# Performance work log

Measured on AMD Instinct MI355X. Metric: run time of the kernel, lower is better.

The kernel has to match this reference:

```python
import jax, jax.numpy as jnp
import numpy as np
from jax import lax

EPS = 1e-5
NUM_GROUPS = 32
OFFSET_SCALE = 1.0
K = 3            # deformable conv kernel size
KK = K * K
DWK = 7          # depthwise kernel size for offset predictor


def group_norm(x, gamma, beta, num_groups=NUM_GROUPS):
    B, C, H, W = x.shape
    xg = x.reshape(B, num_groups, C // num_groups, H, W)
    m = xg.mean(axis=(2, 3, 4), keepdims=True)
    v = xg.var(axis=(2, 3, 4), keepdims=True)
    xn = ((xg - m) * lax.rsqrt(v + EPS)).reshape(B, C, H, W)
    return xn * gamma[None, :, None, None] + beta[None, :, None, None]


def bilinear_gather(x, py, px):
    # x: [B,C,H,W]; py, px: [B,KK,H,W] absolute sample coords -> [B,C,KK,H,W]
    B, C, H, W = x.shape
    y0 = jnp.floor(py)
    x0 = jnp.floor(px)
    wy1 = py - y0
    wx1 = px - x0
    wy0 = 1.0 - wy1
    wx0 = 1.0 - wx1
    xf = x.reshape(B, C, H * W)

    def gather(yi, xi):
        valid = (yi >= 0) & (yi <= H - 1) & (xi >= 0) & (xi <= W - 1)
        yc = jnp.clip(yi, 0, H - 1).astype(jnp.int32)
        xc = jnp.clip(xi, 0, W - 1).astype(jnp.int32)
        idx = (yc * W + xc).reshape(B, -1)                      # [B, KK*H*W]
        g = jax.vmap(lambda a, i: a[:, i])(xf, idx)             # [B, C, KK*H*W]
        g = g.reshape(B, C, KK, H, W)
        return g * valid.astype(x.dtype)[:, None]

    out = (gather(y0, x0) * (wy0 * wx0)[:, None]
           + gather(y0, x0 + 1.0) * (wy0 * wx1)[:, None]
           + gather(y0 + 1.0, x0) * (wy1 * wx0)[:, None]
           + gather(y0 + 1.0, x0 + 1.0) * (wy1 * wx1)[:, None])
    return out


def deform_conv(x, dw, pw, pwb, w, b):
    # x: [B,C,H,W]; dw: [C,1,DWK,DWK] depthwise; pw: [2*KK,C,1,1]; w: [O,C,K,K]
    B, C, H, W = x.shape
    dn = ('NCHW', 'OIHW', 'NCHW')
    f = lax.conv_general_dilated(x, dw, (1, 1), 'SAME',
                                 feature_group_count=C, dimension_numbers=dn)
    off = lax.conv_general_dilated(f, pw, (1, 1), 'SAME', dimension_numbers=dn)
    off = (off + pwb[None, :, None, None]) * OFFSET_SCALE       # [B,2*KK,H,W]
    off = off.reshape(B, KK, 2, H, W)
    ks = jnp.arange(K, dtype=x.dtype) - (K - 1) / 2             # [-1,0,1]
    ky = jnp.repeat(ks, K)                                      # [KK]
    kx = jnp.tile(ks, K)
    yy, xx = jnp.meshgrid(jnp.arange(H, dtype=x.dtype),
                          jnp.arange(W, dtype=x.dtype), indexing='ij')
    py = yy[None, None] + ky[None, :, None, None] + off[:, :, 0]  # [B,KK,H,W]
    px = xx[None, None] + kx[None, :, None, None] + off[:, :, 1]
    sampled = bilinear_gather(x, py, px)                        # [B,C,KK,H,W]
    O = w.shape[0]
    out = jnp.einsum('bckhw,ock->bohw', sampled, w.reshape(O, C, KK))
    return out + b[None, :, None, None]


def setup_inputs() -> dict:
    key = jax.random.key(0)
    ks = jax.random.split(key, 10)
    B, C, H, W = 4, 256, 64, 64
    O = C
    x = jax.random.normal(ks[0], (B, C, H, W), dtype=jnp.float32)

    def conv_w(k, shape, fan_in):
        return jax.random.normal(k, shape, dtype=jnp.float32) / np.sqrt(fan_in)

    inp = {
        'x': x,
        'gn1_g': jnp.ones((C,), jnp.float32), 'gn1_b': jnp.zeros((C,), jnp.float32),
        'dw1': conv_w(ks[1], (C, 1, DWK, DWK), DWK * DWK),
        'pw1': jax.random.normal(ks[2], (2 * KK, C, 1, 1), jnp.float32) * 0.01,
        'pwb1': jnp.zeros((2 * KK,), jnp.float32),
        'w1': conv_w(ks[3], (O, C, K, K), C * KK),
        'b1': jnp.zeros((O,), jnp.float32),
        'gn2_g': jnp.ones((O,), jnp.float32), 'gn2_b': jnp.zeros((O,), jnp.float32),
        'dw2': conv_w(ks[4], (O, 1, DWK, DWK), DWK * DWK),
        'pw2': jax.random.normal(ks[5], (2 * KK, O, 1, 1), jnp.float32) * 0.01,
        'pwb2': jnp.zeros((2 * KK,), jnp.float32),
        'w2': conv_w(ks[6], (O, O, K, K), O * KK),
        'b2': jnp.zeros((O,), jnp.float32),
    }
    return inp


def reference(x, gn1_g, gn1_b, dw1, pw1, pwb1, w1, b1,
              gn2_g, gn2_b, dw2, pw2, pwb2, w2, b2):
    h = jax.nn.relu(group_norm(x, gn1_g, gn1_b))
    h = deform_conv(h, dw1, pw1, pwb1, w1, b1)
    h = jax.nn.relu(group_norm(h, gn2_g, gn2_b))
    # Dropout / DropPath are identity in eval mode
    h = deform_conv(h, dw2, pw2, pwb2, w2, b2)
    return h + x  # shortcut is Identity (in_channels == out_channels)
```

## Files before the change

kernel.cpp:

```cpp
#include <hip/hip_runtime.h>

#define B_    4
#define C_    256
#define H_    64
#define W_    64
#define HW_   4096
#define NG_   32
#define CPG_  8
#define KK_   9
#define NOFF_ 18

typedef __attribute__((ext_vector_type(8))) short short8;
typedef __attribute__((ext_vector_type(4))) short short4v;
typedef __attribute__((ext_vector_type(4))) float floatx4;
typedef __attribute__((ext_vector_type(16))) float floatx16;

static __device__ __forceinline__ short f2bf(float f) {
    union { float f; unsigned u; } v; v.f = f;
    unsigned r = v.u + 0x7fff + ((v.u >> 16) & 1);
    return (short)(r >> 16);
}
static __device__ __forceinline__ float bf2f(short s) {
    union { unsigned u; float f; } v;
    v.u = ((unsigned)(unsigned short)s) << 16;
    return v.f;
}
static __device__ __forceinline__ unsigned pkbf(float lo, float hi) {
    unsigned r;
    asm("v_cvt_pk_bf16_f32 %0, %1, %2" : "=v"(r) : "v"(lo), "v"(hi));
    return r;
}

__global__ __launch_bounds__(1024) void gn_relu_f32_kernel(
    const float* __restrict__ in, const float* __restrict__ gamma,
    const float* __restrict__ beta, short* __restrict__ outb)
{
    int b = blockIdx.x >> 5;
    int g = blockIdx.x & 31;
    const int N = CPG_ * HW_;
    size_t base = ((size_t)(b * C_ + g * CPG_)) * HW_;
    const float4* in4 = (const float4*)(in + base);
    int t = threadIdx.x;

    float s = 0.f, ss = 0.f;
    for (int i = t; i < N / 4; i += 1024) {
        float4 v = in4[i];
        s  += v.x + v.y + v.z + v.w;
        ss += v.x * v.x + v.y * v.y + v.z * v.z + v.w * v.w;
    }
    #pragma unroll
    for (int off = 32; off > 0; off >>= 1) {
        s  += __shfl_down(s, off, 64);
        ss += __shfl_down(ss, off, 64);
    }
    __shared__ float red[32];
    __shared__ float sh_rs, sh_m;
    int wid = t >> 6;
    if ((t & 63) == 0) { red[wid] = s; red[16 + wid] = ss; }
    __syncthreads();
    if (t == 0) {
        float S = 0.f, SS = 0.f;
        #pragma unroll
        for (int i = 0; i < 16; ++i) { S += red[i]; SS += red[16 + i]; }
        float m = S / (float)N;
        float var = SS / (float)N - m * m;
        sh_rs = rsqrtf(var + 1e-5f);
        sh_m = m;
    }
    __syncthreads();
    float rs = sh_rs, m = sh_m;
    short4v* out4 = (short4v*)(outb + base);
    for (int i = t; i < N / 4; i += 1024) {
        int ch = g * CPG_ + (i >> 10);
        float ga = gamma[ch] * rs;
        float be = beta[ch] - m * ga;
        float4 v = in4[i];
        short4v o;
        o.x = f2bf(fmaxf(fmaf(v.x, ga, be), 0.f));
        o.y = f2bf(fmaxf(fmaf(v.y, ga, be), 0.f));
        o.z = f2bf(fmaxf(fmaf(v.z, ga, be), 0.f));
        o.w = f2bf(fmaxf(fmaf(v.w, ga, be), 0.f));
        out4[i] = o;
    }
}

__global__ __launch_bounds__(1024) void gn_relu_bf16_kernel(
    const short* __restrict__ in, const float* __restrict__ gamma,
    const float* __restrict__ beta, short* __restrict__ outb)
{
    int b = blockIdx.x >> 5;
    int g = blockIdx.x & 31;
    const int N = CPG_ * HW_;
    size_t base = ((size_t)(b * C_ + g * CPG_)) * HW_;
    const short4v* in4 = (const short4v*)(in + base);
    int t = threadIdx.x;

    float s = 0.f, ss = 0.f;
    for (int i = t; i < N / 4; i += 1024) {
        short4v sv = in4[i];
        float vx = bf2f(sv.x), vy = bf2f(sv.y), vz = bf2f(sv.z), vw = bf2f(sv.w);
        s  += vx + vy + vz + vw;
        ss += vx * vx + vy * vy + vz * vz + vw * vw;
    }
    #pragma unroll
    for (int off = 32; off > 0; off >>= 1) {
        s  += __shfl_down(s, off, 64);
        ss += __shfl_down(ss, off, 64);
    }
    __shared__ float red[32];
    __shared__ float sh_rs, sh_m;
    int wid = t >> 6;
    if ((t & 63) == 0) { red[wid] = s; red[16 + wid] = ss; }
    __syncthreads();
    if (t == 0) {
        float S = 0.f, SS = 0.f;
        #pragma unroll
        for (int i = 0; i < 16; ++i) { S += red[i]; SS += red[16 + i]; }
        float m = S / (float)N;
        float var = SS / (float)N - m * m;
        sh_rs = rsqrtf(var + 1e-5f);
        sh_m = m;
    }
    __syncthreads();
    float rs = sh_rs, m = sh_m;
    short4v* out4 = (short4v*)(outb + base);
    for (int i = t; i < N / 4; i += 1024) {
        int ch = g * CPG_ + (i >> 10);
        float ga = gamma[ch] * rs;
        float be = beta[ch] - m * ga;
        short4v sv = in4[i];
        short4v o;
        o.x = f2bf(fmaxf(fmaf(bf2f(sv.x), ga, be), 0.f));
        o.y = f2bf(fmaxf(fmaf(bf2f(sv.y), ga, be), 0.f));
        o.z = f2bf(fmaxf(fmaf(bf2f(sv.z), ga, be), 0.f));
        o.w = f2bf(fmaxf(fmaf(bf2f(sv.w), ga, be), 0.f));
        out4[i] = o;
    }
}

__global__ __launch_bounds__(256) void dw7_kernel(
    const short* __restrict__ in, const float* __restrict__ dwk,
    short* __restrict__ out)
{
    int plane = blockIdx.x;
    int c = plane & (C_ - 1);
    const short* src = in + (size_t)plane * HW_;
    short* dst = out + (size_t)plane * HW_;
    __shared__ float tile[70 * 72];
    __shared__ float wk[49];
    int t = threadIdx.x;
    if (t < 49) wk[t] = dwk[c * 49 + t];
    for (int i = t; i < 70 * 72; i += 256) tile[i] = 0.f;
    __syncthreads();
    const short4v* src4 = (const short4v*)src;
    for (int i = t; i < HW_ / 4; i += 256) {
        short4v v = src4[i];
        int y = i >> 4, x = (i & 15) * 4;
        float* tp = &tile[(y + 3) * 72 + (x + 3)];
        tp[0] = bf2f(v.x); tp[1] = bf2f(v.y);
        tp[2] = bf2f(v.z); tp[3] = bf2f(v.w);
    }
    __syncthreads();
    #pragma unroll
    for (int it = 0; it < 4; ++it) {
        int idx = it * 256 + t;
        int y = idx >> 4;
        int x0 = (idx & 15) * 4;
        float a0 = 0.f, a1 = 0.f, a2 = 0.f, a3 = 0.f;
        #pragma unroll
        for (int dy = 0; dy < 7; ++dy) {
            const float* tr = &tile[(y + dy) * 72 + x0];
            float4 ra = *(const float4*)tr;
            float4 rb = *(const float4*)(tr + 4);
            float4 rc = *(const float4*)(tr + 8);
            float r[12] = {ra.x, ra.y, ra.z, ra.w,
                           rb.x, rb.y, rb.z, rb.w,
                           rc.x, rc.y, rc.z, rc.w};
            const float* wr = &wk[dy * 7];
            #pragma unroll
            for (int dx = 0; dx < 7; ++dx) {
                float wv = wr[dx];
                a0 = fmaf(r[dx], wv, a0);
                a1 = fmaf(r[dx + 1], wv, a1);
                a2 = fmaf(r[dx + 2], wv, a2);
                a3 = fmaf(r[dx + 3], wv, a3);
            }
        }
        short4v o;
        o.x = f2bf(a0); o.y = f2bf(a1); o.z = f2bf(a2); o.w = f2bf(a3);
        *(short4v*)&dst[y * 64 + x0] = o;
    }
}

__global__ __launch_bounds__(256) void transpose2_kernel(
    const short* __restrict__ srcA, short* __restrict__ dstA,
    const short* __restrict__ srcB, short* __restrict__ dstB)
{
    int blk = blockIdx.x;
    int h = blk >> 8;
    const short* src = h ? srcB : srcA;
    short*       dst = h ? dstB : dstA;
    int q0 = blk & 255;
    int q = ((q0 & 7) << 5) | (q0 >> 3);
    int b = q >> 6;
    int px0 = (q & 63) * 64;
    __shared__ unsigned ltile[64 * 132];
    int t = threadIdx.x;
    const short* sb = src + (size_t)b * C_ * HW_;

    int pq4 = t & 15, cphi = t >> 4;
    #pragma unroll
    for (int i = 0; i < 8; ++i) {
        int cp = i * 16 + cphi;
        const short* r0 = sb + (size_t)(2 * cp) * HW_ + px0 + pq4 * 4;
        short4v lo = *(const short4v*)r0;
        short4v hi = *(const short4v*)(r0 + HW_);
        #pragma unroll
        for (int j = 0; j < 4; ++j) {
            int pl = pq4 * 4 + j;
            unsigned wrd = (unsigned)(unsigned short)lo[j]
                         | ((unsigned)(unsigned short)hi[j] << 16);
            ltile[pl * 132 + (cp ^ ((pl & 7) << 2))] = wrd;
        }
    }
    __syncthreads();

    int co = t & 31, ph = t >> 5;
    #pragma unroll
    for (int r = 0; r < 8; ++r) {
        int pl = r * 8 + ph;
        uint4 v = *(const uint4*)&ltile[pl * 132 + ((co * 4) ^ ((pl & 7) << 2))];
        *(uint4*)(dst + ((size_t)b * HW_ + px0 + pl) * C_ + co * 8) = v;
    }
}

__global__ __launch_bounds__(256) void wpack_all_kernel(
    const float* __restrict__ w1, const float* __restrict__ w2,
    const float* __restrict__ pw1, const float* __restrict__ pw2,
    short* __restrict__ wp1, short* __restrict__ wp2,
    short* __restrict__ ppk1, short* __restrict__ ppk2)
{
    int blk = blockIdx.x;
    if (blk < 4608) {
        const float* w = (blk < 2304) ? w1 : w2;
        short* wp = (blk < 2304) ? wp1 : wp2;
        int idx = (blk % 2304) * 256 + threadIdx.x;
        int j    = idx & 7;
        int lane = (idx >> 3) & 63;
        int ot   = (idx >> 9) & 7;
        int slab = idx >> 12;
        int g = slab >> 4, cc16 = slab & 15;
        int o = ot * 32 + (lane & 31);
        int c = cc16 * 16 + (lane >> 5) * 8 + j;
        wp[idx] = f2bf(w[(size_t)(o * C_ + c) * KK_ + g]);
    } else {
        int q = blk - 4608;
        const float* pw = (q < 32) ? pw1 : pw2;
        short* ppk = (q < 32) ? ppk1 : ppk2;
        int idx = (q & 31) * 256 + threadIdx.x;
        int j = idx & 7, lane = (idx >> 3) & 63;
        int ot = (idx >> 9) & 1, sl = idx >> 10;
        int o = ot * 16 + (lane & 15);
        int k = sl * 32 + (lane >> 4) * 8 + j;
        ppk[idx] = (o < NOFF_) ? f2bf(pw[o * C_ + k]) : (short)0;
    }
}

__global__ __launch_bounds__(1024, 4) void deform_fused_kernel(
    const short* __restrict__ ht,   const short* __restrict__ fdw,
    const short* __restrict__ ppk,  const float* __restrict__ pwb,
    const short* __restrict__ wp,   const float* __restrict__ bias,
    const float* __restrict__ resid, float* __restrict__ outf,
    short* __restrict__ outb)
{
    int lb = ((blockIdx.x & 7) << 5) | (blockIdx.x >> 3);
    int b = lb >> 6;
    int row = lb & 63;
    __shared__ int   i00[576], i01[576], i10[576], i11[576];
    __shared__ float c00[576], c01[576], c10[576], c11[576];
    __shared__ __align__(16) short sbuf[2][2][8192];
    float* off_lds = (float*)&sbuf[0][0][0];
    int t = threadIdx.x;
    int wv = t >> 6, lane = t & 63;
    int pq = lane >> 4, pr = lane & 15;
    int l31 = lane & 31, hi = lane >> 5;

    if (wv < 8) {
        int ot = wv & 1, ptw = wv >> 1;
        int px = ptw * 16 + pr;
        const short8* fb8 = (const short8*)(fdw +
            ((size_t)b * HW_ + row * 64 + px) * C_);
        const short8* ap = (const short8*)ppk;
        floatx4 pacc = (floatx4){0.f, 0.f, 0.f, 0.f};
        #pragma unroll
        for (int sl = 0; sl < 8; ++sl) {
            short8 af = ap[(sl * 2 + ot) * 64 + lane];
            short8 bf = fb8[sl * 4 + pq];
            pacc = __builtin_amdgcn_mfma_f32_16x16x32_bf16(af, bf, pacc, 0, 0, 0);
        }
        #pragma unroll
        for (int r = 0; r < 4; ++r) {
            int o = ot * 16 + pq * 4 + r;
            if (o < NOFF_) off_lds[o * 64 + px] = pacc[r] + pwb[o];
        }
    }
    __syncthreads();

    if (t < 576) {
        int e = t;
        int k = e >> 6, p = e & 63;
        float offy = off_lds[(2 * k) * 64 + p];
        float offx = off_lds[(2 * k + 1) * 64 + p];
        float py = (float)row + (float)(k / 3 - 1) + offy;
        float px = (float)p   + (float)(k % 3 - 1) + offx;
        float y0f = floorf(py), x0f = floorf(px);
        float wy1 = py - y0f, wx1 = px - x0f;
        float wy0 = 1.f - wy1, wx0 = 1.f - wx1;
        float y1f = y0f + 1.f, x1f = x0f + 1.f;
        bool vy0 = (y0f >= 0.f) && (y0f <= 63.f);
        bool vy1 = (y1f >= 0.f) && (y1f <= 63.f);
        bool vx0 = (x0f >= 0.f) && (x0f <= 63.f);
        bool vx1 = (x1f >= 0.f) && (x1f <= 63.f);
        int iy0 = (int)fminf(fmaxf(y0f, 0.f), 63.f);
        int iy1 = (int)fminf(fmaxf(y1f, 0.f), 63.f);
        int ix0 = (int)fminf(fmaxf(x0f, 0.f), 63.f);
        int ix1 = (int)fminf(fmaxf(x1f, 0.f), 63.f);
        i00[e] = iy0 * 64 + ix0; i01[e] = iy0 * 64 + ix1;
        i10[e] = iy1 * 64 + ix0; i11[e] = iy1 * 64 + ix1;
        c00[e] = (vy0 && vx0) ? wy0 * wx0 : 0.f;
        c01[e] = (vy0 && vx1) ? wy0 * wx1 : 0.f;
        c10[e] = (vy1 && vx0) ? wy1 * wx0 : 0.f;
        c11[e] = (vy1 && vx1) ? wy1 * wx1 : 0.f;
    }
    __syncthreads();

    int c8a = t & 7;
    int pan = (t >> 3) & 1;
    int spx = t >> 4;
    const short* hb = ht + ((size_t)b * HW_) * C_ + pan * 128 + c8a * 8;
    const short* hb0 = hb;
    const short* hb1 = hb + 64;
    int slotA = (c8a ^ (spx & 15)) * 8;
    int slotB = ((c8a + 8) ^ (spx & 15)) * 8;
    int srow = spx * 128;

    short8 ra[4], rb[4];
    auto prefetch = [&](int g) {
        int e = g * 64 + spx;
        int a00 = i00[e], a01 = i01[e], a10 = i10[e], a11 = i11[e];
        ra[0] = *(const short8*)(hb0 + (size_t)a00 * C_);
        ra[1] = *(const short8*)(hb0 + (size_t)a01 * C_);
        ra[2] = *(const short8*)(hb0 + (size_t)a10 * C_);
        ra[3] = *(const short8*)(hb0 + (size_t)a11 * C_);
        rb[0] = *(const short8*)(hb1 + (size_t)a00 * C_);
        rb[1] = *(const short8*)(hb1 + (size_t)a01 * C_);
        rb[2] = *(const short8*)(hb1 + (size_t)a10 * C_);
        rb[3] = *(const short8*)(hb1 + (size_t)a11 * C_);
    };
    auto stage_write = [&](int g, int bi) {
        int e = g * 64 + spx;
        float w00 = c00[e], w01 = c01[e], w10 = c10[e], w11 = c11[e];
        uint4 va, vb;
        float f0, f1;
        #define BLEND(R, J) (w00 * bf2f(R[0][J]) + w01 * bf2f(R[1][J]) \
                           + w10 * bf2f(R[2][J]) + w11 * bf2f(R[3][J]))
        f0 = BLEND(ra, 0); f1 = BLEND(ra, 1); va.x = pkbf(f0, f1);
        f0 = BLEND(ra, 2); f1 = BLEND(ra, 3); va.y = pkbf(f0, f1);
        f0 = BLEND(ra, 4); f1 = BLEND(ra, 5); va.z = pkbf(f0, f1);
        f0 = BLEND(ra, 6); f1 = BLEND(ra, 7); va.w = pkbf(f0, f1);
        f0 = BLEND(rb, 0); f1 = BLEND(rb, 1); vb.x = pkbf(f0, f1);
        f0 = BLEND(rb, 2); f1 = BLEND(rb, 3); vb.y = pkbf(f0, f1);
        f0 = BLEND(rb, 4); f1 = BLEND(rb, 5); vb.z = pkbf(f0, f1);
        f0 = BLEND(rb, 6); f1 = BLEND(rb, 7); vb.w = pkbf(f0, f1);
        #undef BLEND
        short* sp = &sbuf[bi][pan][srow];
        *(uint4*)&sp[slotA] = va;
        *(uint4*)&sp[slotB] = vb;
    };

    int pairId = wv & 7;
    int half = wv >> 3;

    floatx16 acc[2];
    #pragma unroll
    for (int i = 0; i < 16; ++i) { acc[0][i] = 0.f; acc[1][i] = 0.f; }

    prefetch(0);
    stage_write(0, 0);
    prefetch(1);
    __syncthreads();

    const short8* wp8 = (const short8*)wp;
    int msk = l31 & 15;

    for (int g = 0; g < 9; ++g) {
        const short* sb = &sbuf[g & 1][half][0];
        #pragma unroll
        for (int q4 = 0; q4 < 2; ++q4) {
            short8 af[4];
            #pragma unroll
            for (int qq = 0; qq < 4; ++qq)
                af[qq] = wp8[(size_t)(((g * 16 + half * 8 + q4 * 4 + qq) * 8 + pairId) * 64 + lane)];
            #pragma unroll
            for (int qq = 0; qq < 4; ++qq) {
                int ksl = q4 * 4 + qq;
                int so = ((((ksl << 1) | hi) ^ msk) << 3);
                short8 b0 = *(const short8*)&sb[l31 * 128 + so];
                short8 b1 = *(const short8*)&sb[(32 + l31) * 128 + so];
                acc[0] = __builtin_amdgcn_mfma_f32_32x32x16_bf16(af[qq], b0, acc[0], 0, 0, 0);
                acc[1] = __builtin_amdgcn_mfma_f32_32x32x16_bf16(af[qq], b1, acc[1], 0, 0, 0);
            }
        }
        if (g + 1 < 9) {
            stage_write(g + 1, (g + 1) & 1);
            if (g + 2 < 9) prefetch(g + 2);
        }
        __syncthreads();
    }

    float* xch = (float*)&sbuf[0][0][0];
    int wreg = (pairId * 2 + half) * 1024;
    floatx16 aw = half ? acc[0] : acc[1];
    floatx4* xq = (floatx4*)xch;
    #pragma unroll
    for (int j = 0; j < 4; ++j) {
        floatx4 v = {aw[j * 4 + 0], aw[j * 4 + 1], aw[j * 4 + 2], aw[j * 4 + 3]};
        xq[(wreg >> 2) + j * 64 + lane] = v;
    }
    __syncthreads();
    int rreg = (pairId * 2 + (half ^ 1)) * 1024;
    floatx16 ac = half ? acc[1] : acc[0];
    #pragma unroll
    for (int j = 0; j < 4; ++j) {
        floatx4 v = xq[(rreg >> 2) + j * 64 + lane];
        ac[j * 4 + 0] += v.x; ac[j * 4 + 1] += v.y;
        ac[j * 4 + 2] += v.z; ac[j * 4 + 3] += v.w;
    }

    #pragma unroll
    for (int r = 0; r < 16; ++r) {
        int o = pairId * 32 + (r & 3) + 8 * (r >> 2) + 4 * hi;
        float v = ac[r] + bias[o];
        size_t ob = ((size_t)(b * C_ + o)) * HW_ + row * 64 + half * 32 + l31;
        if (outf) {
            if (resid) v += resid[ob];
            outf[ob] = v;
        } else {
            outb[ob] = f2bf(v);
        }
    }
}

extern "C" void kernel_launch(void* const* d_in, const int* in_sizes, int n_in,
                              void* d_out, int out_size, void* d_ws, size_t ws_size,
                              hipStream_t stream)
{
    const float* x     = (const float*)d_in[0];
    const float* gn1_g = (const float*)d_in[1];
    const float* gn1_b = (const float*)d_in[2];
    const float* dw1   = (const float*)d_in[3];
    const float* pw1   = (const float*)d_in[4];
    const float* pwb1  = (const float*)d_in[5];
    const float* w1    = (const float*)d_in[6];
    const float* b1    = (const float*)d_in[7];
    const float* gn2_g = (const float*)d_in[8];
    const float* gn2_b = (const float*)d_in[9];
    const float* dw2   = (const float*)d_in[10];
    const float* pw2   = (const float*)d_in[11];
    const float* pwb2  = (const float*)d_in[12];
    const float* w2    = (const float*)d_in[13];
    const float* b2    = (const float*)d_in[14];
    float* out = (float*)d_out;

    float* ws   = (float*)d_ws;
    short* y1b  = (short*)ws;
    short* hbf  = (short*)(ws + 2097152);
    short* hbt  = (short*)(ws + 4194304);
    short* fdwc = (short*)(ws + 6291456);
    short* fdwt = (short*)(ws + 8388608);
    short* wp1  = (short*)(ws + 10485760);
    short* wp2  = (short*)(ws + 10780672);
    short* ppk1 = (short*)(ws + 11075584);
    short* ppk2 = (short*)(ws + 11079680);

    wpack_all_kernel<<<4672, 256, 0, stream>>>(w1, w2, pw1, pw2,
                                               wp1, wp2, ppk1, ppk2);

    gn_relu_f32_kernel<<<B_ * NG_, 1024, 0, stream>>>(x, gn1_g, gn1_b, hbf);
    dw7_kernel<<<B_ * C_, 256, 0, stream>>>(hbf, dw1, fdwc);
    transpose2_kernel<<<512, 256, 0, stream>>>(hbf, hbt, fdwc, fdwt);
    deform_fused_kernel<<<B_ * H_, 1024, 0, stream>>>(
        hbt, fdwt, ppk1, pwb1, wp1, b1, nullptr, nullptr, y1b);

    gn_relu_bf16_kernel<<<B_ * NG_, 1024, 0, stream>>>(y1b, gn2_g, gn2_b, hbf);
    dw7_kernel<<<B_ * C_, 256, 0, stream>>>(hbf, dw2, fdwc);
    transpose2_kernel<<<512, 256, 0, stream>>>(hbf, hbt, fdwc, fdwt);
    deform_fused_kernel<<<B_ * H_, 1024, 0, stream>>>(
        hbt, fdwt, ppk2, pwb2, wp2, b2, x, out, nullptr);
}
```

Measured before the change: 246.4 us.

## Fuse depthwise 7x7 conv with transpose and switch to channel-octet blocked layout

Merges the depthwise 7x7 conv and the NCHW-to-NHWC transpose into one launch. Half the blocks compute the depthwise conv for 8 channels over half an image and write the result straight into a blocked [b][pixel-row][c/8][px][8] layout. The other half transpose the activations into a [b][c/8][pixel][8] layout. The deform kernel's gather and offset-predictor loads are rewritten for these layouts. This removes the intermediate depthwise output round trip through memory and one kernel launch per stage. The cost is a large LDS footprint (about 78 KB) that may limit occupancy, and gather loads now stride across channel-octet planes.

After: 288.0 us. +16.9%, slower.

```diff
diff --git a/kernel.cpp b/kernel.cpp
--- a/kernel.cpp
+++ b/kernel.cpp
@@ -138,99 +138,105 @@
     }
 }
 
-__global__ __launch_bounds__(256) void dw7_kernel(
-    const short* __restrict__ in, const float* __restrict__ dwk,
-    short* __restrict__ out)
+__global__ __launch_bounds__(256) void dw7t_tr_kernel(
+    const short* __restrict__ in,
+    const float* __restrict__ dwk,
+    short* __restrict__ fdwt,
+    short* __restrict__ ht)
 {
-    int plane = blockIdx.x;
-    int c = plane & (C_ - 1);
-    const short* src = in + (size_t)plane * HW_;
-    short* dst = out + (size_t)plane * HW_;
-    __shared__ float tile[70 * 72];
-    __shared__ float wk[49];
+    __shared__ __align__(16) char smem[78112];
     int t = threadIdx.x;
-    if (t < 49) wk[t] = dwk[c * 49 + t];
-    for (int i = t; i < 70 * 72; i += 256) tile[i] = 0.f;
-    __syncthreads();
-    const short4v* src4 = (const short4v*)src;
-    for (int i = t; i < HW_ / 4; i += 256) {
-        short4v v = src4[i];
-        int y = i >> 4, x = (i & 15) * 4;
-        float* tp = &tile[(y + 3) * 72 + (x + 3)];
-        tp[0] = bf2f(v.x); tp[1] = bf2f(v.y);
-        tp[2] = bf2f(v.z); tp[3] = bf2f(v.w);
-    }
-    __syncthreads();
-    #pragma unroll
-    for (int it = 0; it < 4; ++it) {
-        int idx = it * 256 + t;
-        int y = idx >> 4;
-        int x0 = (idx & 15) * 4;
-        float a0 = 0.f, a1 = 0.f, a2 = 0.f, a3 = 0.f;
-        #pragma unroll
-        for (int dy = 0; dy < 7; ++dy) {
-            const float* tr = &tile[(y + dy) * 72 + x0];
-            float4 ra = *(const float4*)tr;
-            float4 rb = *(const float4*)(tr + 4);
-            float4 rc = *(const float4*)(tr + 8);
-            float r[12] = {ra.x, ra.y, ra.z, ra.w,
-                           rb.x, rb.y, rb.z, rb.w,
-                           rc.x, rc.y, rc.z, rc.w};
-            const float* wr = &wk[dy * 7];
+    int blk = blockIdx.x;
+    if (blk < 256) {
+        short (*tile)[38][72] = (short(*)[38][72])smem;
+        float (*wk8)[49]      = (float(*)[49])(smem + 43776);
+        short (*outs)[2048]   = (short(*)[2048])(smem + 45344);
+        int b = blk >> 6, o8 = (blk >> 1) & 31, rh = blk & 1;
+        int c0 = o8 * 8;
+        unsigned* tz = (unsigned*)smem;
+        for (int i = t; i < 10944; i += 256) tz[i] = 0u;
+        for (int i = t; i < 392; i += 256)
+            wk8[i / 49][i % 49] = dwk[(c0 + i / 49) * 49 + (i % 49)];
+        __syncthreads();
+        for (int ch = 0; ch < 8; ++ch) {
+            const short* src = in + ((size_t)(b * C_ + c0 + ch)) * HW_;
+            for (int i = t; i < 608; i += 256) {
+                int rr = i >> 4, xq = i & 15;
+                int ry = rh * 32 + rr - 3;
+                if (ry >= 0 && ry < 64) {
+                    short4v v = *(const short4v*)(src + ry * 64 + xq * 4);
+                    *(short4v*)&tile[ch][rr][4 + xq * 4] = v;
+                }
+            }
+        }
+        __syncthreads();
+        for (int it = 0; it < 16; ++it) {
+            int q = it * 256 + t;
+            int ch = q >> 9, y = (q >> 4) & 31, x0 = (q & 15) << 2;
+            float a0 = 0.f, a1 = 0.f, a2 = 0.f, a3 = 0.f;
+            const float* wr0 = wk8[ch];
             #pragma unroll
-            for (int dx = 0; dx < 7; ++dx) {
-                float wv = wr[dx];
-                a0 = fmaf(r[dx], wv, a0);
-                a1 = fmaf(r[dx + 1], wv, a1);
-                a2 = fmaf(r[dx + 2], wv, a2);
-                a3 = fmaf(r[dx + 3], wv, a3);
+            for (int dy = 0; dy < 7; ++dy) {
+                const short* trw = &tile[ch][y + dy][x0];
+                short4v s0 = *(const short4v*)trw;
+                short4v s1 = *(const short4v*)(trw + 4);
+                short4v s2 = *(const short4v*)(trw + 8);
+                float r[12] = {bf2f(s0.x), bf2f(s0.y), bf2f(s0.z), bf2f(s0.w),
+                               bf2f(s1.x), bf2f(s1.y), bf2f(s1.z), bf2f(s1.w),
+                               bf2f(s2.x), bf2f(s2.y), bf2f(s2.z), bf2f(s2.w)};
+                const float* wr = wr0 + dy * 7;
+                #pragma unroll
+                for (int dx = 0; dx < 7; ++dx) {
+                    float wv = wr[dx];
+                    a0 = fmaf(r[dx + 1], wv, a0);
+                    a1 = fmaf(r[dx + 2], wv, a1);
+                    a2 = fmaf(r[dx + 3], wv, a2);
+                    a3 = fmaf(r[dx + 4], wv, a3);
+                }
             }
-        }
-        short4v o;
-        o.x = f2bf(a0); o.y = f2bf(a1); o.z = f2bf(a2); o.w = f2bf(a3);
-        *(short4v*)&dst[y * 64 + x0] = o;
-    }
-}
-
-__global__ __launch_bounds__(256) void transpose2_kernel(
-    const short* __restrict__ srcA, short* __restrict__ dstA,
-    const short* __restrict__ srcB, short* __restrict__ dstB)
-{
-    int blk = blockIdx.x;
-    int h = blk >> 8;
-    const short* src = h ? srcB : srcA;
-    short*       dst = h ? dstB : dstA;
-    int q0 = blk & 255;
-    int q = ((q0 & 7) << 5) | (q0 >> 3);
-    int b = q >> 6;
-    int px0 = (q & 63) * 64;
-    __shared__ unsigned ltile[64 * 132];
-    int t = threadIdx.x;
-    const short* sb = src + (size_t)b * C_ * HW_;
-
-    int pq4 = t & 15, cphi = t >> 4;
-    #pragma unroll
-    for (int i = 0; i < 8; ++i) {
-        int cp = i * 16 + cphi;
-        const short* r0 = sb + (size_t)(2 * cp) * HW_ + px0 + pq4 * 4;
-        short4v lo = *(const short4v*)r0;
-        short4v hi = *(const short4v*)(r0 + HW_);
-        #pragma unroll
-        for (int j = 0; j < 4; ++j) {
-            int pl = pq4 * 4 + j;
-            unsigned wrd = (unsigned)(unsigned short)lo[j]
-                         | ((unsigned)(unsigned short)hi[j] << 16);
-            ltile[pl * 132 + (cp ^ ((pl & 7) << 2))] = wrd;
-        }
-    }
-    __syncthreads();
-
-    int co = t & 31, ph = t >> 5;
-    #pragma unroll
-    for (int r = 0; r < 8; ++r) {
-        int pl = r * 8 + ph;
-        uint4 v = *(const uint4*)&ltile[pl * 132 + ((co * 4) ^ ((pl & 7) << 2))];
-        *(uint4*)(dst + ((size_t)b * HW_ + px0 + pl) * C_ + co * 8) = v;
+            short4v o;
+            o.x = f2bf(a0); o.y = f2bf(a1); o.z = f2bf(a2); o.w = f2bf(a3);
+            *(short4v*)&outs[ch][y * 64 + x0] = o;
+        }
+        __syncthreads();
+        for (int it = 0; it < 8; ++it) {
+            int p = it * 256 + t;
+            short8 v;
+            #pragma unroll
+            for (int ch = 0; ch < 8; ++ch) v[ch] = outs[ch][p];
+            *(short8*)(fdwt + (((size_t)(b * 64 + rh * 32 + (p >> 6)) * 32 + o8) * 64
+                               + (p & 63)) * 8) = v;
+        }
+    } else {
+        unsigned* ltile = (unsigned*)smem;
+        int q0 = blk - 256;
+        int q = ((q0 & 7) << 5) | (q0 >> 3);
+        int b = q >> 6;
+        int px0 = (q & 63) * 64;
+        const short* sb = in + (size_t)b * C_ * HW_;
+        int pq4 = t & 15, cphi = t >> 4;
+        #pragma unroll
+        for (int i = 0; i < 8; ++i) {
+            int cp = i * 16 + cphi;
+            const short* r0 = sb + (size_t)(2 * cp) * HW_ + px0 + pq4 * 4;
+            short4v lo = *(const short4v*)r0;
+            short4v hi = *(const short4v*)(r0 + HW_);
+            #pragma unroll
+            for (int j = 0; j < 4; ++j) {
+                int pl = pq4 * 4 + j;
+                unsigned wrd = (unsigned)(unsigned short)lo[j]
+                             | ((unsigned)(unsigned short)hi[j] << 16);
+                ltile[pl * 132 + (cp ^ ((pl & 7) << 2))] = wrd;
+            }
+        }
+        __syncthreads();
+        int pl = t & 63, coq = t >> 6;
+        #pragma unroll
+        for (int r = 0; r < 8; ++r) {
+            int co = r * 4 + coq;
+            uint4 v = *(const uint4*)&ltile[pl * 132 + ((co * 4) ^ ((pl & 7) << 2))];
+            *(uint4*)(ht + ((size_t)(b * 32 + co) * HW_ + px0 + pl) * 8) = v;
+        }
     }
 }
 
@@ -288,14 +294,14 @@
     if (wv < 8) {
         int ot = wv & 1, ptw = wv >> 1;
         int px = ptw * 16 + pr;
-        const short8* fb8 = (const short8*)(fdw +
-            ((size_t)b * HW_ + row * 64 + px) * C_);
+        const short8* fdw8 = (const short8*)fdw;
+        size_t fbase = ((size_t)(b * 64 + row)) * 32;
         const short8* ap = (const short8*)ppk;
         floatx4 pacc = (floatx4){0.f, 0.f, 0.f, 0.f};
         #pragma unroll
         for (int sl = 0; sl < 8; ++sl) {
             short8 af = ap[(sl * 2 + ot) * 64 + lane];
-            short8 bf = fb8[sl * 4 + pq];
+            short8 bf = fdw8[(fbase + sl * 4 + pq) * 64 + px];
             pacc = __builtin_amdgcn_mfma_f32_16x16x32_bf16(af, bf, pacc, 0, 0, 0);
         }
         #pragma unroll
@@ -337,9 +343,9 @@
     int c8a = t & 7;
     int pan = (t >> 3) & 1;
     int spx = t >> 4;
-    const short* hb = ht + ((size_t)b * HW_) * C_ + pan * 128 + c8a * 8;
-    const short* hb0 = hb;
-    const short* hb1 = hb + 64;
+    const short8* ht8 = (const short8*)ht;
+    size_t gbase0 = ((size_t)(b * 32 + pan * 16 + c8a)) * HW_;
+    size_t gbase1 = ((size_t)(b * 32 + pan * 16 + c8a + 8)) * HW_;
     int slotA = (c8a ^ (spx & 15)) * 8;
     int slotB = ((c8a + 8) ^ (spx & 15)) * 8;
     int srow = spx * 128;
@@ -348,14 +354,14 @@
     auto prefetch = [&](int g) {
         int e = g * 64 + spx;
         int a00 = i00[e], a01 = i01[e], a10 = i10[e], a11 = i11[e];
-        ra[0] = *(const short8*)(hb0 + (size_t)a00 * C_);
-        ra[1] = *(const short8*)(hb0 + (size_t)a01 * C_);
-        ra[2] = *(const short8*)(hb0 + (size_t)a10 * C_);
-        ra[3] = *(const short8*)(hb0 + (size_t)a11 * C_);
-        rb[0] = *(const short8*)(hb1 + (size_t)a00 * C_);
-        rb[1] = *(const short8*)(hb1 + (size_t)a01 * C_);
-        rb[2] = *(const short8*)(hb1 + (size_t)a10 * C_);
-        rb[3] = *(const short8*)(hb1 + (size_t)a11 * C_);
+        ra[0] = ht8[gbase0 + a00];
+        ra[1] = ht8[gbase0 + a01];
+        ra[2] = ht8[gbase0 + a10];
+        ra[3] = ht8[gbase0 + a11];
+        rb[0] = ht8[gbase1 + a00];
+        rb[1] = ht8[gbase1 + a01];
+        rb[2] = ht8[gbase1 + a10];
+        rb[3] = ht8[gbase1 + a11];
     };
     auto stage_write = [&](int g, int bi) {
         int e = g * 64 + spx;
@@ -476,7 +482,6 @@
     short* y1b  = (short*)ws;
     short* hbf  = (short*)(ws + 2097152);
     short* hbt  = (short*)(ws + 4194304);
-    short* fdwc = (short*)(ws + 6291456);
     short* fdwt = (short*)(ws + 8388608);
     short* wp1  = (short*)(ws + 10485760);
     short* wp2  = (short*)(ws + 10780672);
@@ -487,14 +492,12 @@
                                                wp1, wp2, ppk1, ppk2);
 
     gn_relu_f32_kernel<<<B_ * NG_, 1024, 0, stream>>>(x, gn1_g, gn1_b, hbf);
-    dw7_kernel<<<B_ * C_, 256, 0, stream>>>(hbf, dw1, fdwc);
-    transpose2_kernel<<<512, 256, 0, stream>>>(hbf, hbt, fdwc, fdwt);
+    dw7t_tr_kernel<<<512, 256, 0, stream>>>(hbf, dw1, fdwt, hbt);
     deform_fused_kernel<<<B_ * H_, 1024, 0, stream>>>(
         hbt, fdwt, ppk1, pwb1, wp1, b1, nullptr, nullptr, y1b);
 
     gn_relu_bf16_kernel<<<B_ * NG_, 1024, 0, stream>>>(y1b, gn2_g, gn2_b, hbf);
-    dw7_kernel<<<B_ * C_, 256, 0, stream>>>(hbf, dw2, fdwc);
-    transpose2_kernel<<<512, 256, 0, stream>>>(hbf, hbt, fdwc, fdwt);
+    dw7t_tr_kernel<<<512, 256, 0, stream>>>(hbf, dw2, fdwt, hbt);
     deform_fused_kernel<<<B_ * H_, 1024, 0, stream>>>(
         hbt, fdwt, ppk2, pwb2, wp2, b2, x, out, nullptr);
 }
```
